# Kernel tuning notes

Hardware: AMD Instinct MI355X
Metric: run time of the kernel (lower is better)

Reference implementation:

```python
import jax, jax.numpy as jnp
import numpy as np

N = 50000      # nodes
E_RAND = 800000
IN = 256       # in_dim
HID = 64       # num_hidden
H = 4          # heads for GATv2 layers 0,1
C = 32         # num_classes (final layer, 1 head)
SLOPE = 0.2


def setup_inputs() -> dict:
    key = jax.random.key(0)
    ks = jax.random.split(key, 12)
    x = jax.random.normal(ks[0], (N, IN), dtype=jnp.float32)
    src = jax.random.randint(ks[1], (E_RAND,), 0, N, dtype=jnp.int32)
    dst = jax.random.randint(ks[2], (E_RAND,), 0, N, dtype=jnp.int32)
    loops = jnp.arange(N, dtype=jnp.int32)  # self-loops: every node has an in-edge
    src = jnp.concatenate([src, loops])
    dst = jnp.concatenate([dst, loops])
    s = 0.05
    W0 = jax.random.normal(ks[3], (IN, H * HID), dtype=jnp.float32) * s
    a0 = jax.random.normal(ks[4], (H, HID), dtype=jnp.float32) * s
    W1 = jax.random.normal(ks[5], (H * HID, H * HID), dtype=jnp.float32) * s
    a1 = jax.random.normal(ks[6], (H, HID), dtype=jnp.float32) * s
    W2 = jax.random.normal(ks[7], (H * HID, 1 * C), dtype=jnp.float32) * s
    a2 = jax.random.normal(ks[8], (1, C), dtype=jnp.float32) * s
    Wres2 = jax.random.normal(ks[9], (H * HID, C), dtype=jnp.float32) * s
    return {"x": x, "src": src, "dst": dst, "W0": W0, "a0": a0,
            "W1": W1, "a1": a1, "W2": W2, "a2": a2, "Wres2": Wres2}


def _gatv2_layer(h, W, a, src, dst, heads, out, res, activation):
    n = h.shape[0]
    # share_weights=True: same projection for src and dst (DGL GATv2Conv)
    f = (h @ W).reshape(n, heads, out)            # [N,H,D]
    fe = f[src] + f[dst]                          # gather: [E,H,D]
    e = jnp.einsum('ehd,hd->eh', jax.nn.leaky_relu(fe, SLOPE), a)  # [E,H]
    # edge softmax over incoming edges per destination node
    m = jax.ops.segment_max(e, dst, num_segments=n)
    ex = jnp.exp(e - m[dst])
    z = jax.ops.segment_sum(ex, dst, num_segments=n)
    alpha = ex / z[dst]                           # [E,H]
    msg = alpha[:, :, None] * f[src]              # [E,H,D]
    rst = jax.ops.segment_sum(msg, dst, num_segments=n)  # [N,H,D]
    if res is not None:
        rst = rst + res
    if activation:
        rst = jax.nn.elu(rst)
    return rst


def reference(x, src, dst, W0, a0, W1, a1, W2, a2, Wres2):
    # layer 0: no residual, elu, flatten heads
    h = _gatv2_layer(x, W0, a0, src, dst, H, HID, None, True).reshape(N, H * HID)
    # layer 1: residual (in == heads*out -> identity reshape), elu, flatten
    res1 = h.reshape(N, H, HID)
    h = _gatv2_layer(h, W1, a1, src, dst, H, HID, res1, True).reshape(N, H * HID)
    # final layer: residual via res_fc (256 != 1*32), no activation, mean over heads
    res2 = (h @ Wres2).reshape(N, 1, C)
    logits = _gatv2_layer(h, W2, a2, src, dst, 1, C, res2, False).mean(axis=1)
    return logits
```

## Files before the change

### kernel.cpp

```cpp
#include <hip/hip_runtime.h>
#include <hip/hip_bf16.h>

typedef __hip_bfloat16 bf16;
#define SLOPE 0.2f

__device__ __forceinline__ float b2f(bf16 v) { return __bfloat162float(v); }
__device__ __forceinline__ short f2b_raw(float x) {
    bf16 b = __float2bfloat16(x);
    return *reinterpret_cast<short*>(&b);
}

typedef __attribute__((ext_vector_type(8))) short bf16x8;
typedef __attribute__((ext_vector_type(16))) float f32x16;
typedef __attribute__((ext_vector_type(2))) float f32x2;

union Q16 { uint4 q[2]; unsigned u[8]; };

__global__ void k_prep(const void* __restrict__ x,
                       const void* __restrict__ W0, const void* __restrict__ W1,
                       const void* __restrict__ W2, const void* __restrict__ Wr2,
                       const void* __restrict__ a0, const void* __restrict__ a1,
                       const void* __restrict__ a2, bf16* __restrict__ W0p,
                       bf16* __restrict__ W1p, bf16* __restrict__ W2fp,
                       bf16* __restrict__ a0c, bf16* __restrict__ a1c,
                       bf16* __restrict__ a2c, int* __restrict__ flag,
                       int* __restrict__ cnt, int* __restrict__ ticket, int N) {
    __shared__ int sflag;
    if (threadIdx.x < 64) {
        const unsigned short* u = (const unsigned short*)x;
        int tid = threadIdx.x;
        int nice = 0;
        for (int k = tid; k < 256; k += 64) {
            unsigned int bits = ((unsigned int)u[2 * k]) << 16;
            float v = __uint_as_float(bits);
            float av = fabsf(v);
            if (v == 0.0f || (av > 1e-6f && av < 100.0f)) ++nice;
        }
        for (int off = 32; off > 0; off >>= 1) nice += __shfl_down(nice, off, 64);
        if (tid == 0) sflag = (nice >= 192) ? 0 : 1;
    }
    __syncthreads();
    int isf = sflag;
    int idx = blockIdx.x * blockDim.x + threadIdx.x;
    if (blockIdx.x == 0 && threadIdx.x == 0) { *flag = isf; *ticket = 0; }
    if (idx < N) cnt[idx] = 0;
    if (idx < 131072) {
        int t = idx & 65535;
        int j = t & 7, L = (t >> 3) & 63, kt = (t >> 9) & 15, nt = t >> 13;
        int n = nt * 32 + (L & 31);
        int k = kt * 16 + (L >> 5) * 8 + j;
        const void* src = (idx < 65536) ? W0 : W1;
        float v = isf ? ((const float*)src)[k * 256 + n] : b2f(((const bf16*)src)[k * 256 + n]);
        bf16* dstp = (idx < 65536) ? W0p : W1p;
        dstp[t] = __float2bfloat16(v);
    } else if (idx < 147456) {
        int t = idx - 131072;
        int j = t & 7, L = (t >> 3) & 63, kt = (t >> 9) & 15, nt = t >> 13;
        int n = nt * 32 + (L & 31);
        int k = kt * 16 + (L >> 5) * 8 + j;
        const void* src = (n < 32) ? W2 : Wr2;
        int nn = n & 31;
        float v = isf ? ((const float*)src)[k * 32 + nn] : b2f(((const bf16*)src)[k * 32 + nn]);
        W2fp[t] = __float2bfloat16(v);
    } else if (idx < 147456 + 256) {
        int t = idx - 147456;
        float v = isf ? ((const float*)a0)[t] : b2f(((const bf16*)a0)[t]);
        a0c[t] = __float2bfloat16(v);
    } else if (idx < 147456 + 512) {
        int t = idx - 147456 - 256;
        float v = isf ? ((const float*)a1)[t] : b2f(((const bf16*)a1)[t]);
        a1c[t] = __float2bfloat16(v);
    } else if (idx < 147456 + 544) {
        int t = idx - 147456 - 512;
        float v = isf ? ((const float*)a2)[t] : b2f(((const bf16*)a2)[t]);
        a2c[t] = __float2bfloat16(v);
    }
}

__global__ void k_hist(const int* __restrict__ dst, int* __restrict__ cnt, int E) {
    int e = blockIdx.x * blockDim.x + threadIdx.x;
    if (e < E) atomicAdd(&cnt[dst[e]], 1);
}

__global__ void k_bsum_scan(const int* __restrict__ cnt, int* __restrict__ bsum,
                            int* __restrict__ ticket, int n, int B) {
    __shared__ int sh[256];
    __shared__ int lastFlag;
    int base = blockIdx.x * 1024 + threadIdx.x * 4;
    int s = 0;
#pragma unroll
    for (int k = 0; k < 4; ++k) { int i = base + k; if (i < n) s += cnt[i]; }
    sh[threadIdx.x] = s;
    __syncthreads();
    for (int off = 128; off > 0; off >>= 1) {
        if (threadIdx.x < off) sh[threadIdx.x] += sh[threadIdx.x + off];
        __syncthreads();
    }
    if (threadIdx.x == 0) {
        atomicExch(&bsum[blockIdx.x], sh[0]);
        __threadfence();
        int t = atomicAdd(ticket, 1);
        lastFlag = (t == B - 1) ? 1 : 0;
    }
    __syncthreads();
    if (lastFlag && threadIdx.x < 64) {
        int tid = threadIdx.x;
        int v = (tid < B) ? atomicAdd(&bsum[tid], 0) : 0;
        int xv = v;
#pragma unroll
        for (int off = 1; off < 64; off <<= 1) {
            int y = __shfl_up(xv, off, 64);
            if (tid >= off) xv += y;
        }
        if (tid < B) bsum[tid] = xv - v;
    }
}

__global__ void k_scanwrite(const int* __restrict__ cnt, const int* __restrict__ bsum,
                            int* __restrict__ rowptr, int* __restrict__ cursor, int n, int E) {
    __shared__ int sh[256];
    int base = blockIdx.x * 1024 + threadIdx.x * 4;
    int loc[4];
    int s = 0;
#pragma unroll
    for (int k = 0; k < 4; ++k) {
        int i = base + k;
        loc[k] = (i < n) ? cnt[i] : 0;
        s += loc[k];
    }
    sh[threadIdx.x] = s;
    __syncthreads();
    for (int off = 1; off < 256; off <<= 1) {
        int u = (threadIdx.x >= off) ? sh[threadIdx.x - off] : 0;
        __syncthreads();
        sh[threadIdx.x] += u;
        __syncthreads();
    }
    int run = bsum[blockIdx.x] + sh[threadIdx.x] - s;
#pragma unroll
    for (int k = 0; k < 4; ++k) {
        int i = base + k;
        if (i < n) { rowptr[i] = run; cursor[i] = run; run += loc[k]; }
    }
    if (blockIdx.x == 0 && threadIdx.x == 0) rowptr[n] = E;
}

__global__ void k_scatter(const int* __restrict__ src, const int* __restrict__ dst,
                          int* __restrict__ cursor, int* __restrict__ csr_src, int E) {
    int e = blockIdx.x * blockDim.x + threadIdx.x;
    if (e < E) {
        int p = atomicAdd(&cursor[dst[e]], 1);
        csr_src[p] = src[e];
    }
}

template <int ADAPT>
__global__ void k_gemm_mfma(const void* __restrict__ A, const bf16* __restrict__ Wp,
                            bf16* __restrict__ C, int Nrows, const int* __restrict__ flag) {
    int warp = threadIdx.x >> 6;
    int lane = threadIdx.x & 63;
    int wr = warp >> 1;
    int wc = warp & 1;
    long rowBase = (long)blockIdx.x * 64 + wr * 32;
    int colBase = wc * 128;
    int m = lane & 31;
    int g = lane >> 5;
    long r = rowBase + m;
    if (r >= Nrows) r = Nrows - 1;
    int isf32 = ADAPT ? *flag : 0;
    const short* Ab = (const short*)A + r * 256 + g * 8;
    const float* Af = (const float*)A + r * 256 + g * 8;
    const short* Wps = (const short*)Wp;
    f32x16 acc[4] = {};
    for (int kt = 0; kt < 16; ++kt) {
        bf16x8 af;
        if (ADAPT && isf32) {
            float4 x0 = *(const float4*)(Af + kt * 16);
            float4 x1 = *(const float4*)(Af + kt * 16 + 4);
            union { bf16x8 v; short s[8]; } t;
            t.s[0] = f2b_raw(x0.x); t.s[1] = f2b_raw(x0.y);
            t.s[2] = f2b_raw(x0.z); t.s[3] = f2b_raw(x0.w);
            t.s[4] = f2b_raw(x1.x); t.s[5] = f2b_raw(x1.y);
            t.s[6] = f2b_raw(x1.z); t.s[7] = f2b_raw(x1.w);
            af = t.v;
        } else {
            af = *(const bf16x8*)(Ab + kt * 16);
        }
#pragma unroll
        for (int ct = 0; ct < 4; ++ct) {
            int nt = wc * 4 + ct;
            bf16x8 bfr = *(const bf16x8*)(Wps + (((nt << 4) + kt) << 9) + lane * 8);
            acc[ct] = __builtin_amdgcn_mfma_f32_32x32x16_bf16(af, bfr, acc[ct], 0, 0, 0);
        }
    }
#pragma unroll
    for (int ct = 0; ct < 4; ++ct) {
#pragma unroll
        for (int i = 0; i < 16; ++i) {
            long row = rowBase + (i & 3) + 8 * (i >> 2) + 4 * g;
            if (row < Nrows)
                C[row * 256 + colBase + ct * 32 + m] = __float2bfloat16(acc[ct][i]);
        }
    }
}

__global__ void k_gemm_mfma64(const bf16* __restrict__ A, const bf16* __restrict__ Wp,
                              bf16* __restrict__ C, int Nrows) {
    int warp = threadIdx.x >> 6;
    int lane = threadIdx.x & 63;
    long rowBase = (long)blockIdx.x * 128 + warp * 32;
    int m = lane & 31;
    int g = lane >> 5;
    long r = rowBase + m;
    if (r >= Nrows) r = Nrows - 1;
    const short* Arow = (const short*)A + r * 256 + g * 8;
    const short* Wps = (const short*)Wp;
    f32x16 acc[2] = {};
    for (int kt = 0; kt < 16; ++kt) {
        bf16x8 af = *(const bf16x8*)(Arow + kt * 16);
#pragma unroll
        for (int ct = 0; ct < 2; ++ct) {
            bf16x8 bfr = *(const bf16x8*)(Wps + (((ct << 4) + kt) << 9) + lane * 8);
            acc[ct] = __builtin_amdgcn_mfma_f32_32x32x16_bf16(af, bfr, acc[ct], 0, 0, 0);
        }
    }
#pragma unroll
    for (int ct = 0; ct < 2; ++ct) {
#pragma unroll
        for (int i = 0; i < 16; ++i) {
            long row = rowBase + (i & 3) + 8 * (i >> 2) + 4 * g;
            if (row < Nrows)
                C[row * 64 + ct * 32 + m] = __float2bfloat16(acc[ct][i]);
        }
    }
}

__global__ void k_gat_fused(const uint4* __restrict__ f, const bf16* __restrict__ a,
                            const int* __restrict__ rowptr, const int* __restrict__ csr_src,
                            const uint4* __restrict__ res, uint4* __restrict__ out,
                            int N, int mode) {
    int n = (blockIdx.x * blockDim.x + threadIdx.x) >> 6;
    int lane = threadIdx.x & 63;
    if (n >= N) return;
    int j = lane >> 4, l = lane & 15;

    Q16 fdq, aq;
    fdq.q[0] = f[(long)n * 32 + 2 * l];
    fdq.q[1] = f[(long)n * 32 + 2 * l + 1];
    aq.q[0] = ((const uint4*)a)[2 * l];
    aq.q[1] = ((const uint4*)a)[2 * l + 1];
    f32x2 fd2[8], a6[8], a4[8];
#pragma unroll
    for (int i = 0; i < 8; ++i) {
        f32x2 fv, av;
        fv.x = __uint_as_float(fdq.u[i] << 16);
        fv.y = __uint_as_float(fdq.u[i] & 0xffff0000u);
        av.x = __uint_as_float(aq.u[i] << 16);
        av.y = __uint_as_float(aq.u[i] & 0xffff0000u);
        fd2[i] = fv;
        a6[i] = 0.6f * av;
        a4[i] = 0.4f * av;
    }

    int p0 = rowptr[n], p1 = rowptr[n + 1];
    int iters = (p1 - p0 + 3) >> 2;
    float z = 0.f;
    f32x2 acc[8] = {};

    int p = p0 + j;
    int pc = p1 - 1;
    Q16 A0, A1, B0, B1;
    {
        int s0 = csr_src[min(p, pc)];
        A0.q[0] = f[(long)s0 * 32 + 2 * l];
        A0.q[1] = f[(long)s0 * 32 + 2 * l + 1];
        int s1 = csr_src[min(p + 4, pc)];
        A1.q[0] = f[(long)s1 * 32 + 2 * l];
        A1.q[1] = f[(long)s1 * 32 + 2 * l + 1];
    }
    for (int i = 0; i < iters; i += 2) {
        int s0 = csr_src[min(p + 8, pc)];
        B0.q[0] = f[(long)s0 * 32 + 2 * l];
        B0.q[1] = f[(long)s0 * 32 + 2 * l + 1];
        int s1 = csr_src[min(p + 12, pc)];
        B1.q[0] = f[(long)s1 * 32 + 2 * l];
        B1.q[1] = f[(long)s1 * 32 + 2 * l + 1];

#pragma unroll
        for (int half = 0; half < 2; ++half) {
            if (half == 1 && i + 1 >= iters) break;
            const Q16& cur = half ? A1 : A0;
            int pp = p + half * 4;
            f32x2 fs[8];
            f32x2 t2 = {0.f, 0.f};
#pragma unroll
            for (int k = 0; k < 8; ++k) {
                f32x2 fv;
                fv.x = __uint_as_float(cur.u[k] << 16);
                fv.y = __uint_as_float(cur.u[k] & 0xffff0000u);
                fs[k] = fv;
                f32x2 u = fv + fd2[k];
                f32x2 ua;
                ua.x = __uint_as_float(__float_as_uint(u.x) & 0x7fffffffu);
                ua.y = __uint_as_float(__float_as_uint(u.y) & 0x7fffffffu);
                t2 = a6[k] * u + t2;
                t2 = a4[k] * ua + t2;
            }
            float t = t2.x + t2.y;
            t += __shfl_xor(t, 1);
            t += __shfl_xor(t, 2);
            float wgt = (pp < p1) ? __expf(t) : 0.f;
            z += wgt;
            f32x2 w2 = {wgt, wgt};
#pragma unroll
            for (int k = 0; k < 8; ++k) acc[k] = w2 * fs[k] + acc[k];
        }
        A0 = B0;
        A1 = B1;
        p += 8;
    }
    z += __shfl_xor(z, 16);
    z += __shfl_xor(z, 32);
#pragma unroll
    for (int k = 0; k < 8; ++k) {
        acc[k].x += __shfl_xor(acc[k].x, 16);
        acc[k].x += __shfl_xor(acc[k].x, 32);
        acc[k].y += __shfl_xor(acc[k].y, 16);
        acc[k].y += __shfl_xor(acc[k].y, 32);
    }
    if (j < 2) {
        float invz = 1.f / z;
        float o[8];
#pragma unroll
        for (int k = 0; k < 4; ++k) {
            int kk = j * 4 + k;
            o[2 * k]     = acc[kk].x * invz;
            o[2 * k + 1] = acc[kk].y * invz;
        }
        if (mode == 1) {
            uint4 rq = res[(long)n * 32 + 2 * l + j];
            const unsigned* ru = (const unsigned*)&rq;
#pragma unroll
            for (int k = 0; k < 4; ++k) {
                o[2 * k]     += __uint_as_float(ru[k] << 16);
                o[2 * k + 1] += __uint_as_float(ru[k] & 0xffff0000u);
            }
        }
        union { uint4 q; short s[8]; } ob;
#pragma unroll
        for (int k = 0; k < 8; ++k) {
            float v = o[k] > 0.f ? o[k] : (__expf(o[k]) - 1.f);
            ob.s[k] = f2b_raw(v);
        }
        out[(long)n * 32 + 2 * l + j] = ob.q;
    }
}

__global__ void k_gat_fused_fin(const unsigned* __restrict__ fr2u, const bf16* __restrict__ a2,
                                const int* __restrict__ rowptr, const int* __restrict__ csr_src,
                                void* __restrict__ outraw, int N, const int* __restrict__ flag) {
    int n = (blockIdx.x * blockDim.x + threadIdx.x) >> 6;
    int lane = threadIdx.x & 63;
    if (n >= N) return;
    int j = lane >> 4, l = lane & 15;

    unsigned fdu = fr2u[(long)n * 32 + l];
    unsigned au  = ((const unsigned*)a2)[l];
    f32x2 fd2, a6, a4;
    fd2.x = __uint_as_float(fdu << 16);
    fd2.y = __uint_as_float(fdu & 0xffff0000u);
    float ax = __uint_as_float(au << 16);
    float ay = __uint_as_float(au & 0xffff0000u);
    a6.x = 0.6f * ax; a6.y = 0.6f * ay;
    a4.x = 0.4f * ax; a4.y = 0.4f * ay;

    int p0 = rowptr[n], p1 = rowptr[n + 1];
    int iters = (p1 - p0 + 3) >> 2;
    float z = 0.f;
    f32x2 acc = {0.f, 0.f};

    int p = p0 + j;
    int pc = p1 - 1;
    unsigned A0, A1, B0, B1;
    A0 = fr2u[(long)csr_src[min(p, pc)] * 32 + l];
    A1 = fr2u[(long)csr_src[min(p + 4, pc)] * 32 + l];
    for (int i = 0; i < iters; i += 2) {
        B0 = fr2u[(long)csr_src[min(p + 8, pc)] * 32 + l];
        B1 = fr2u[(long)csr_src[min(p + 12, pc)] * 32 + l];
#pragma unroll
        for (int half = 0; half < 2; ++half) {
            if (half == 1 && i + 1 >= iters) break;
            unsigned cu = half ? A1 : A0;
            int pp = p + half * 4;
            f32x2 fs;
            fs.x = __uint_as_float(cu << 16);
            fs.y = __uint_as_float(cu & 0xffff0000u);
            f32x2 u = fs + fd2;
            f32x2 ua;
            ua.x = __uint_as_float(__float_as_uint(u.x) & 0x7fffffffu);
            ua.y = __uint_as_float(__float_as_uint(u.y) & 0x7fffffffu);
            f32x2 t2 = a6 * u + a4 * ua;
            float t = t2.x + t2.y;
            t += __shfl_xor(t, 1);
            t += __shfl_xor(t, 2);
            t += __shfl_xor(t, 4);
            t += __shfl_xor(t, 8);
            float wgt = (pp < p1) ? __expf(t) : 0.f;
            z += wgt;
            f32x2 w2 = {wgt, wgt};
            acc = w2 * fs + acc;
        }
        A0 = B0;
        A1 = B1;
        p += 8;
    }
    z += __shfl_xor(z, 16);
    z += __shfl_xor(z, 32);
    acc.x += __shfl_xor(acc.x, 16);
    acc.x += __shfl_xor(acc.x, 32);
    acc.y += __shfl_xor(acc.y, 16);
    acc.y += __shfl_xor(acc.y, 32);
    if (j == 0) {
        unsigned ru = fr2u[(long)n * 32 + 16 + l];
        float invz = 1.f / z;
        float o0 = acc.x * invz + __uint_as_float(ru << 16);
        float o1 = acc.y * invz + __uint_as_float(ru & 0xffff0000u);
        if (*flag) {
            float2 ov = {o0, o1};
            ((float2*)outraw)[(long)n * 16 + l] = ov;
        } else {
            unsigned ob = ((unsigned)(unsigned short)f2b_raw(o0)) |
                          (((unsigned)(unsigned short)f2b_raw(o1)) << 16);
            ((unsigned*)outraw)[(long)n * 16 + l] = ob;
        }
    }
}

extern "C" void kernel_launch(void* const* d_in, const int* in_sizes, int n_in,
                              void* d_out, int out_size, void* d_ws, size_t ws_size,
                              hipStream_t stream) {
    const int N = in_sizes[0] / 256;
    const int E = in_sizes[1];

    const void* x   = d_in[0];
    const int*  src = (const int*)d_in[1];
    const int*  dst = (const int*)d_in[2];

    char* w = (char*)d_ws;
    auto alloc = [&](size_t bytes) -> char* {
        char* p = w;
        w += (bytes + 15) & ~(size_t)15;
        return p;
    };
    bf16* buf0 = (bf16*)alloc((size_t)N * 256 * 2);
    bf16* buf1 = (bf16*)alloc((size_t)N * 256 * 2);
    bf16* buf2 = (bf16*)alloc((size_t)N * 256 * 2);
    int* csr_src = (int*)alloc((size_t)E * 4);
    int* rowptr  = (int*)alloc((size_t)(N + 1) * 4);
    int* cursor  = (int*)alloc((size_t)N * 4);
    int* cnt     = (int*)alloc((size_t)N * 4);
    int* bsum    = (int*)alloc((size_t)1024 * 4);
    bf16* W0p  = (bf16*)alloc((size_t)65536 * 2);
    bf16* W1p  = (bf16*)alloc((size_t)65536 * 2);
    bf16* W2fp = (bf16*)alloc((size_t)64 * 256 * 2);
    bf16* a0c  = (bf16*)alloc((size_t)256 * 2);
    bf16* a1c  = (bf16*)alloc((size_t)256 * 2);
    bf16* a2c  = (bf16*)alloc((size_t)32 * 2);
    int*  flag = (int*)alloc(16);
    int*  ticket = (int*)alloc(16);

    bf16* hA  = buf1;
    bf16* fB  = buf2;
    bf16* hB  = buf0;
    bf16* fr2 = buf2;

    int prepN = 147456 + 544;
    if (prepN < N) prepN = N;
    k_prep<<<(prepN + 255) / 256, 256, 0, stream>>>(
        x, d_in[3], d_in[5], d_in[7], d_in[9], d_in[4], d_in[6], d_in[8],
        W0p, W1p, W2fp, a0c, a1c, a2c, flag, cnt, ticket, N);

    const int B = (N + 1023) / 1024;
    k_hist<<<(E + 255) / 256, 256, 0, stream>>>(dst, cnt, E);
    k_bsum_scan<<<B, 256, 0, stream>>>(cnt, bsum, ticket, N, B);
    k_scanwrite<<<B, 256, 0, stream>>>(cnt, bsum, rowptr, cursor, N, E);
    k_scatter<<<(E + 255) / 256, 256, 0, stream>>>(src, dst, cursor, csr_src, E);

    const int ngrid4 = (int)(((long)N * 64 + 255) / 256);

    k_gemm_mfma<1><<<(N + 63) / 64, 256, 0, stream>>>(x, W0p, fB, N, flag);
    k_gat_fused<<<ngrid4, 256, 0, stream>>>((const uint4*)fB, a0c, rowptr, csr_src,
                                            nullptr, (uint4*)hA, N, 0);
    k_gemm_mfma<0><<<(N + 63) / 64, 256, 0, stream>>>(hA, W1p, fB, N, flag);
    k_gat_fused<<<ngrid4, 256, 0, stream>>>((const uint4*)fB, a1c, rowptr, csr_src,
                                            (const uint4*)hA, (uint4*)hB, N, 1);
    k_gemm_mfma64<<<(N + 127) / 128, 256, 0, stream>>>(hB, W2fp, fr2, N);
    k_gat_fused_fin<<<ngrid4, 256, 0, stream>>>((const unsigned*)fr2, a2c, rowptr, csr_src,
                                                d_out, N, flag);
}
```

Baseline: 435.1 us.

## Fuse histogram into prep kernel and merge scan kernels with spin-wait

```diff
diff --git a/kernel.cpp b/kernel.cpp
--- a/kernel.cpp
+++ b/kernel.cpp
@@ -24,7 +24,8 @@
                        bf16* __restrict__ W1p, bf16* __restrict__ W2fp,
                        bf16* __restrict__ a0c, bf16* __restrict__ a1c,
                        bf16* __restrict__ a2c, int* __restrict__ flag,
-                       int* __restrict__ cnt, int* __restrict__ ticket, int N) {
+                       int* __restrict__ ticket, int* __restrict__ done,
+                       const int* __restrict__ dste, int* __restrict__ cnt, int E) {
     __shared__ int sflag;
     if (threadIdx.x < 64) {
         const unsigned short* u = (const unsigned short*)x;
@@ -42,8 +43,8 @@
     __syncthreads();
     int isf = sflag;
     int idx = blockIdx.x * blockDim.x + threadIdx.x;
-    if (blockIdx.x == 0 && threadIdx.x == 0) { *flag = isf; *ticket = 0; }
-    if (idx < N) cnt[idx] = 0;
+    if (blockIdx.x == 0 && threadIdx.x == 0) { *flag = isf; *ticket = 0; *done = 0; }
+    if (idx < E) atomicAdd(&cnt[dste[idx]], 1);
     if (idx < 131072) {
         int t = idx & 65535;
         int j = t & 7, L = (t >> 3) & 63, kt = (t >> 9) & 15, nt = t >> 13;
@@ -77,48 +78,12 @@
     }
 }
 
-__global__ void k_hist(const int* __restrict__ dst, int* __restrict__ cnt, int E) {
-    int e = blockIdx.x * blockDim.x + threadIdx.x;
-    if (e < E) atomicAdd(&cnt[dst[e]], 1);
-}
-
-__global__ void k_bsum_scan(const int* __restrict__ cnt, int* __restrict__ bsum,
-                            int* __restrict__ ticket, int n, int B) {
+__global__ void k_scan_fused(const int* __restrict__ cnt, int* __restrict__ bsum,
+                             int* __restrict__ bscan, int* __restrict__ ticket,
+                             int* __restrict__ done, int* __restrict__ rowptr,
+                             int* __restrict__ cursor, int n, int E, int B) {
     __shared__ int sh[256];
-    __shared__ int lastFlag;
-    int base = blockIdx.x * 1024 + threadIdx.x * 4;
-    int s = 0;
-#pragma unroll
-    for (int k = 0; k < 4; ++k) { int i = base + k; if (i < n) s += cnt[i]; }
-    sh[threadIdx.x] = s;
-    __syncthreads();
-    for (int off = 128; off > 0; off >>= 1) {
-        if (threadIdx.x < off) sh[threadIdx.x] += sh[threadIdx.x + off];
-        __syncthreads();
-    }
-    if (threadIdx.x == 0) {
-        atomicExch(&bsum[blockIdx.x], sh[0]);
-        __threadfence();
-        int t = atomicAdd(ticket, 1);
-        lastFlag = (t == B - 1) ? 1 : 0;
-    }
-    __syncthreads();
-    if (lastFlag && threadIdx.x < 64) {
-        int tid = threadIdx.x;
-        int v = (tid < B) ? atomicAdd(&bsum[tid], 0) : 0;
-        int xv = v;
-#pragma unroll
-        for (int off = 1; off < 64; off <<= 1) {
-            int y = __shfl_up(xv, off, 64);
-            if (tid >= off) xv += y;
-        }
-        if (tid < B) bsum[tid] = xv - v;
-    }
-}
-
-__global__ void k_scanwrite(const int* __restrict__ cnt, const int* __restrict__ bsum,
-                            int* __restrict__ rowptr, int* __restrict__ cursor, int n, int E) {
-    __shared__ int sh[256];
+    __shared__ int sbase;
     int base = blockIdx.x * 1024 + threadIdx.x * 4;
     int loc[4];
     int s = 0;
@@ -136,7 +101,32 @@
         sh[threadIdx.x] += u;
         __syncthreads();
     }
-    int run = bsum[blockIdx.x] + sh[threadIdx.x] - s;
+    if (threadIdx.x == 0) {
+        atomicExch(&bsum[blockIdx.x], sh[255]);
+        __threadfence();
+        int t = atomicAdd(ticket, 1);
+        sbase = (t == B - 1) ? 1 : 0;
+    }
+    __syncthreads();
+    if (sbase && threadIdx.x < 64) {
+        int tid = threadIdx.x;
+        int v = (tid < B) ? atomicAdd(&bsum[tid], 0) : 0;
+        int xv = v;
+#pragma unroll
+        for (int off = 1; off < 64; off <<= 1) {
+            int y = __shfl_up(xv, off, 64);
+            if (tid >= off) xv += y;
+        }
+        if (tid < B) atomicExch(&bscan[tid], xv - v);
+        __threadfence();
+        if (tid == 0) atomicExch(done, 1);
+    }
+    if (threadIdx.x == 0) {
+        while (atomicAdd(done, 0) == 0) {}
+        sbase = atomicAdd(&bscan[blockIdx.x], 0);
+    }
+    __syncthreads();
+    int run = sbase + sh[threadIdx.x] - s;
 #pragma unroll
     for (int k = 0; k < 4; ++k) {
         int i = base + k;
@@ -152,6 +142,7 @@
         int p = atomicAdd(&cursor[dst[e]], 1);
         csr_src[p] = src[e];
     }
+    if (e < 32) csr_src[E + e] = 0;
 }
 
 template <int ADAPT>
@@ -268,21 +259,20 @@
     f32x2 acc[8] = {};
 
     int p = p0 + j;
-    int pc = p1 - 1;
     Q16 A0, A1, B0, B1;
     {
-        int s0 = csr_src[min(p, pc)];
+        int s0 = csr_src[p];
         A0.q[0] = f[(long)s0 * 32 + 2 * l];
         A0.q[1] = f[(long)s0 * 32 + 2 * l + 1];
-        int s1 = csr_src[min(p + 4, pc)];
+        int s1 = csr_src[p + 4];
         A1.q[0] = f[(long)s1 * 32 + 2 * l];
         A1.q[1] = f[(long)s1 * 32 + 2 * l + 1];
     }
     for (int i = 0; i < iters; i += 2) {
-        int s0 = csr_src[min(p + 8, pc)];
+        int s0 = csr_src[p + 8];
         B0.q[0] = f[(long)s0 * 32 + 2 * l];
         B0.q[1] = f[(long)s0 * 32 + 2 * l + 1];
-        int s1 = csr_src[min(p + 12, pc)];
+        int s1 = csr_src[p + 12];
         B1.q[0] = f[(long)s1 * 32 + 2 * l];
         B1.q[1] = f[(long)s1 * 32 + 2 * l + 1];
 
@@ -380,13 +370,12 @@
     f32x2 acc = {0.f, 0.f};
 
     int p = p0 + j;
-    int pc = p1 - 1;
     unsigned A0, A1, B0, B1;
-    A0 = fr2u[(long)csr_src[min(p, pc)] * 32 + l];
-    A1 = fr2u[(long)csr_src[min(p + 4, pc)] * 32 + l];
+    A0 = fr2u[(long)csr_src[p] * 32 + l];
+    A1 = fr2u[(long)csr_src[p + 4] * 32 + l];
     for (int i = 0; i < iters; i += 2) {
-        B0 = fr2u[(long)csr_src[min(p + 8, pc)] * 32 + l];
-        B1 = fr2u[(long)csr_src[min(p + 12, pc)] * 32 + l];
+        B0 = fr2u[(long)csr_src[p + 8] * 32 + l];
+        B1 = fr2u[(long)csr_src[p + 12] * 32 + l];
 #pragma unroll
         for (int half = 0; half < 2; ++half) {
             if (half == 1 && i + 1 >= iters) break;
@@ -455,11 +444,12 @@
     bf16* buf0 = (bf16*)alloc((size_t)N * 256 * 2);
     bf16* buf1 = (bf16*)alloc((size_t)N * 256 * 2);
     bf16* buf2 = (bf16*)alloc((size_t)N * 256 * 2);
-    int* csr_src = (int*)alloc((size_t)E * 4);
+    int* csr_src = (int*)alloc((size_t)(E + 32) * 4);
     int* rowptr  = (int*)alloc((size_t)(N + 1) * 4);
     int* cursor  = (int*)alloc((size_t)N * 4);
     int* cnt     = (int*)alloc((size_t)N * 4);
-    int* bsum    = (int*)alloc((size_t)1024 * 4);
+    int* bsum    = (int*)alloc((size_t)128 * 4);
+    int* bscan   = (int*)alloc((size_t)128 * 4);
     bf16* W0p  = (bf16*)alloc((size_t)65536 * 2);
     bf16* W1p  = (bf16*)alloc((size_t)65536 * 2);
     bf16* W2fp = (bf16*)alloc((size_t)64 * 256 * 2);
@@ -468,22 +458,22 @@
     bf16* a2c  = (bf16*)alloc((size_t)32 * 2);
     int*  flag = (int*)alloc(16);
     int*  ticket = (int*)alloc(16);
+    int*  done = (int*)alloc(16);
 
     bf16* hA  = buf1;
     bf16* fB  = buf2;
     bf16* hB  = buf0;
     bf16* fr2 = buf2;
 
+    hipMemsetAsync(cnt, 0, (size_t)N * 4, stream);
     int prepN = 147456 + 544;
-    if (prepN < N) prepN = N;
+    if (prepN < E) prepN = E;
     k_prep<<<(prepN + 255) / 256, 256, 0, stream>>>(
         x, d_in[3], d_in[5], d_in[7], d_in[9], d_in[4], d_in[6], d_in[8],
-        W0p, W1p, W2fp, a0c, a1c, a2c, flag, cnt, ticket, N);
+        W0p, W1p, W2fp, a0c, a1c, a2c, flag, ticket, done, dst, cnt, E);
 
     const int B = (N + 1023) / 1024;
-    k_hist<<<(E + 255) / 256, 256, 0, stream>>>(dst, cnt, E);
-    k_bsum_scan<<<B, 256, 0, stream>>>(cnt, bsum, ticket, N, B);
-    k_scanwrite<<<B, 256, 0, stream>>>(cnt, bsum, rowptr, cursor, N, E);
+    k_scan_fused<<<B, 256, 0, stream>>>(cnt, bsum, bscan, ticket, done, rowptr, cursor, N, E, B);
     k_scatter<<<(E + 255) / 256, 256, 0, stream>>>(src, dst, cursor, csr_src, E);
 
     const int ngrid4 = (int)(((long)N * 64 + 255) / 256);
```

Result: no change. 441.8 us (+1.5%).
